# Performance work log

Measured on AMD Instinct MI355X. Metric: run time of the kernel, lower is better.

## Reference

```python
import jax, jax.numpy as jnp
import numpy as np

D_MODEL = 2048
N_HEADS = 32
N_KV_HEADS = 8
HEAD_DIM = D_MODEL // N_HEADS
ROPE_BASE = 10000.0

def setup_inputs() -> dict:
    key = jax.random.key(0)
    ks = jax.random.split(key, 5)
    B, S = 1, 2048
    x = jax.random.normal(ks[0], (B, S, D_MODEL), dtype=jnp.float32)
    sc = 1.0 / np.sqrt(D_MODEL)
    Wq = jax.random.normal(ks[1], (D_MODEL, D_MODEL), dtype=jnp.float32) * sc
    Wk = jax.random.normal(ks[2], (N_KV_HEADS * HEAD_DIM, D_MODEL), dtype=jnp.float32) * sc
    Wv = jax.random.normal(ks[3], (N_KV_HEADS * HEAD_DIM, D_MODEL), dtype=jnp.float32) * sc
    Wo = jax.random.normal(ks[4], (D_MODEL, D_MODEL), dtype=jnp.float32) * sc
    return {"x": x, "Wq": Wq, "Wk": Wk, "Wv": Wv, "Wo": Wo}

def _rope_cos_sin(seq_len, dtype):
    inv_freq = 1.0 / (ROPE_BASE ** (jnp.arange(0, HEAD_DIM, 2, dtype=jnp.float32) / HEAD_DIM))
    t = jnp.arange(seq_len, dtype=jnp.float32)
    freqs = jnp.einsum('i,j->ij', t, inv_freq)          # [S, hd/2]
    emb = jnp.concatenate([freqs, freqs], axis=-1)      # [S, hd]
    return jnp.cos(emb).astype(dtype), jnp.sin(emb).astype(dtype)

def _rotate_half(x):
    x1, x2 = x[..., : HEAD_DIM // 2], x[..., HEAD_DIM // 2 :]
    return jnp.concatenate([-x2, x1], axis=-1)

def reference(x, Wq, Wk, Wv, Wo):
    B, S, _ = x.shape
    scale = HEAD_DIM ** -0.5
    # projections (Linear: x @ W.T)
    q = (x @ Wq.T).reshape(B, S, N_HEADS, HEAD_DIM).transpose(0, 2, 1, 3)      # [B,H,S,hd]
    k = (x @ Wk.T).reshape(B, S, N_KV_HEADS, HEAD_DIM).transpose(0, 2, 1, 3)   # [B,Hkv,S,hd]
    v = (x @ Wv.T).reshape(B, S, N_KV_HEADS, HEAD_DIM).transpose(0, 2, 1, 3)
    cos, sin = _rope_cos_sin(S, x.dtype)                # [S,hd], broadcasts over B,H
    q = q * cos + _rotate_half(q) * sin
    k = k * cos + _rotate_half(k) * sin
    rep = N_HEADS // N_KV_HEADS
    k = jnp.repeat(k, rep, axis=1)                       # [B,H,S,hd]
    v = jnp.repeat(v, rep, axis=1)
    scores = jnp.einsum('bhqd,bhkd->bhqk', q, k) * scale # [B,H,S,S]
    attn = jax.nn.softmax(scores, axis=-1)
    out = jnp.einsum('bhqk,bhkd->bhqd', attn, v)         # [B,H,S,hd]
    out = out.transpose(0, 2, 1, 3).reshape(B, S, D_MODEL)
    return out @ Wo.T
```

## Files before the change

### kernel.cpp

```cpp
#include <hip/hip_runtime.h>
#include <hip/hip_bf16.h>
#include <cmath>

typedef __bf16 bf16_t;
typedef __attribute__((ext_vector_type(8))) __bf16 bf16x8;
typedef __attribute__((ext_vector_type(4))) float f32x4;
typedef __attribute__((ext_vector_type(4))) short s16x4;

#define S_LEN 2048
#define DMODEL 2048
#define KVDIM 512
#define NHEADS 32
#define NKV 8
#define HDIM 64

__device__ inline f32x4 zero4() { f32x4 z; z[0]=0.f; z[1]=0.f; z[2]=0.f; z[3]=0.f; return z; }

__global__ void convert_all(const float* __restrict__ s0, bf16_t* __restrict__ d0,
                            const float* __restrict__ s1, bf16_t* __restrict__ d1,
                            const float* __restrict__ s2, bf16_t* __restrict__ d2,
                            const float* __restrict__ s3, bf16_t* __restrict__ d3,
                            const float* __restrict__ s4, bf16_t* __restrict__ d4) {
  int b = blockIdx.x;
  const float* src; bf16_t* dst; int boff;
  if      (b < 2048) { src = s0; dst = d0; boff = b; }
  else if (b < 4096) { src = s1; dst = d1; boff = b - 2048; }
  else if (b < 4608) { src = s2; dst = d2; boff = b - 4096; }
  else if (b < 5120) { src = s3; dst = d3; boff = b - 4608; }
  else               { src = s4; dst = d4; boff = b - 5120; }
  int idx = (boff * 256 + threadIdx.x) * 8;
  bf16x8 v;
#pragma unroll
  for (int j = 0; j < 8; j++) v[j] = (bf16_t)src[idx + j];
  *(bf16x8*)(dst + idx) = v;
}

template <int BN, bool F32OUT>
__device__ __forceinline__ void gemm_core(const bf16_t* __restrict__ A,
                                          const bf16_t* __restrict__ Bt,
                                          void* __restrict__ Cout,
                                          int N, int K, int bm, int bn) {
  constexpr int NT_W = BN / 32;
  __shared__ __attribute__((aligned(16))) bf16_t As[128 * 64];
  __shared__ __attribute__((aligned(16))) bf16_t Bs[BN * 64];
  const int tid  = threadIdx.x;
  const int wave = tid >> 6, lane = tid & 63;
  const int wm = wave >> 1, wn = wave & 1;
  const int quad = lane >> 4, lr = lane & 15;
  const int srow = lane >> 3, scol = lane & 7;

  f32x4 acc[4][NT_W];
#pragma unroll
  for (int i = 0; i < 4; i++)
#pragma unroll
    for (int j = 0; j < NT_W; j++) acc[i][j] = zero4();

  for (int k0 = 0; k0 < K; k0 += 64) {
#pragma unroll
    for (int i = 0; i < 4; i++) {
      const bf16_t* gA = A + (size_t)(bm + i * 32 + wave * 8 + srow) * K + k0 + scol * 8;
      bf16_t* lA = As + (i * 32 + wave * 8) * 64;
      __builtin_amdgcn_global_load_lds((const __attribute__((address_space(1))) void*)gA,
                                       (__attribute__((address_space(3))) void*)lA, 16, 0, 0);
    }
#pragma unroll
    for (int i = 0; i < BN / 32; i++) {
      const bf16_t* gB = Bt + (size_t)(bn + i * 32 + wave * 8 + srow) * K + k0 + scol * 8;
      bf16_t* lB = Bs + (i * 32 + wave * 8) * 64;
      __builtin_amdgcn_global_load_lds((const __attribute__((address_space(1))) void*)gB,
                                       (__attribute__((address_space(3))) void*)lB, 16, 0, 0);
    }
    __syncthreads();
#pragma unroll
    for (int ks = 0; ks < 2; ks++) {
      bf16x8 a[4], b[NT_W];
#pragma unroll
      for (int mt = 0; mt < 4; mt++)
        a[mt] = *(const bf16x8*)&As[(wm * 64 + mt * 16 + lr) * 64 + ks * 32 + quad * 8];
#pragma unroll
      for (int nt = 0; nt < NT_W; nt++)
        b[nt] = *(const bf16x8*)&Bs[(wn * (BN / 2) + nt * 16 + lr) * 64 + ks * 32 + quad * 8];
#pragma unroll
      for (int mt = 0; mt < 4; mt++)
#pragma unroll
        for (int nt = 0; nt < NT_W; nt++)
          acc[mt][nt] = __builtin_amdgcn_mfma_f32_16x16x32_bf16(a[mt], b[nt], acc[mt][nt], 0, 0, 0);
    }
    __syncthreads();
  }

#pragma unroll
  for (int mt = 0; mt < 4; mt++)
#pragma unroll
    for (int nt = 0; nt < NT_W; nt++)
#pragma unroll
      for (int r = 0; r < 4; r++) {
        int row = bm + wm * 64 + mt * 16 + quad * 4 + r;
        int col = bn + wn * (BN / 2) + nt * 16 + lr;
        if (F32OUT) ((float*)Cout)[(size_t)row * N + col] = acc[mt][nt][r];
        else ((bf16_t*)Cout)[(size_t)row * N + col] = (bf16_t)acc[mt][nt][r];
      }
}

__global__ __launch_bounds__(256) void gemm_proj(const bf16_t* __restrict__ xb,
                                                 const bf16_t* __restrict__ Wqb,
                                                 const bf16_t* __restrict__ Wkb,
                                                 const bf16_t* __restrict__ Wvb,
                                                 bf16_t* __restrict__ qb,
                                                 bf16_t* __restrict__ kb,
                                                 bf16_t* __restrict__ vb) {
  int b = blockIdx.x;
  if (b < 512) {
    gemm_core<64, false>(xb, Wqb, qb, 2048, 2048, (b >> 5) * 128, (b & 31) * 64);
  } else if (b < 640) {
    int r = b - 512;
    gemm_core<64, false>(xb, Wkb, kb, 512, 2048, (r >> 3) * 128, (r & 7) * 64);
  } else {
    int r = b - 640;
    gemm_core<64, false>(Wvb, xb, vb, 2048, 2048, (r >> 5) * 128, (r & 31) * 64);
  }
}

__global__ __launch_bounds__(256) void gemm_out(const bf16_t* __restrict__ A,
                                                const bf16_t* __restrict__ Bt,
                                                float* __restrict__ C) {
  int b = blockIdx.x;
  gemm_core<64, true>(A, Bt, C, 2048, 2048, (b >> 5) * 128, (b & 31) * 64);
}

__global__ void rope_k(bf16_t* __restrict__ kb) {
  int idx = blockIdx.x * 256 + threadIdx.x;
  int s = idx >> 8;
  int rem = idx & 255;
  int head = rem >> 5;
  int i = rem & 31;
  float freq = __expf(-0.2878231366f * (float)i);
  float ang = (float)s * freq;
  float sn, cs;
  sincosf(ang, &sn, &cs);
  size_t base = (size_t)s * KVDIM + head * 64 + i;
  float x0 = (float)kb[base];
  float x1 = (float)kb[base + 32];
  kb[base]      = (bf16_t)(x0 * cs - x1 * sn);
  kb[base + 32] = (bf16_t)(x1 * cs + x0 * sn);
}

__global__ __launch_bounds__(256) void attn_kernel(const bf16_t* __restrict__ q,
                                                   const bf16_t* __restrict__ k,
                                                   const bf16_t* __restrict__ vT,
                                                   bf16_t* __restrict__ out) {
  __shared__ __attribute__((aligned(16))) bf16_t Ks[128 * 64];
  __shared__ __attribute__((aligned(16))) bf16_t Vs[64 * 128];
  const int tid  = threadIdx.x;
  const int wave = tid >> 6, lane = tid & 63;
  const int quad = lane >> 4, lr = lane & 15;
  const int srow = lane >> 3, scol = lane & 7;
  const int vrow = lane >> 4, vcol = lane & 15;
  const int cg = scol ^ srow;
  const int qt = blockIdx.x, h = blockIdx.y;
  const int hkv = h >> 2;
  const int qrow0 = qt * 128 + wave * 32;
  const int sw = lr & 7;
  const int c0 = (quad ^ sw) * 8;
  const int c1 = ((quad + 4) ^ sw) * 8;

  bf16x8 aqA0, aqA1, aqB0, aqB1;
#pragma unroll
  for (int set = 0; set < 2; set++) {
    int row = qrow0 + set * 16 + lr;
    const bf16_t* qp = q + (size_t)row * DMODEL + h * HDIM + quad * 8;
    bf16x8 r0 = *(const bf16x8*)qp;
    bf16x8 r1 = *(const bf16x8*)(qp + 32);
    float srow_f = (float)row;
    bf16x8 a0, a1;
#pragma unroll
    for (int j = 0; j < 8; j++) {
      float freq = __expf(-0.2878231366f * (float)(quad * 8 + j));
      float sn, cs;
      sincosf(srow_f * freq, &sn, &cs);
      float x0 = (float)r0[j], x1 = (float)r1[j];
      a0[j] = (bf16_t)(x0 * cs - x1 * sn);
      a1[j] = (bf16_t)(x1 * cs + x0 * sn);
    }
    if (set == 0) { aqA0 = a0; aqA1 = a1; } else { aqB0 = a0; aqB1 = a1; }
  }

  f32x4 OA[4], OB[4];
  float lA = 0.f, lB = 0.f;
#pragma unroll
  for (int mt = 0; mt < 4; mt++) { OA[mt] = zero4(); OB[mt] = zero4(); }

  for (int kt = 0; kt < S_LEN; kt += 128) {
#pragma unroll
    for (int j = 0; j < 4; j++) {
      const bf16_t* gK = k + (size_t)(kt + wave * 32 + j * 8 + srow) * KVDIM + hkv * HDIM + cg * 8;
      bf16_t* lK = Ks + (wave * 32 + j * 8) * 64;
      __builtin_amdgcn_global_load_lds((const __attribute__((address_space(1))) void*)gK,
                                       (__attribute__((address_space(3))) void*)lK, 16, 0, 0);
    }
#pragma unroll
    for (int j = 0; j < 4; j++) {
      int dg = wave * 16 + j * 4 + vrow;
      int cgv = vcol ^ (dg & 7);
      const bf16_t* gV = vT + (size_t)(hkv * HDIM + dg) * S_LEN + kt + cgv * 8;
      bf16_t* lV = Vs + (wave * 16 + j * 4) * 128;
      __builtin_amdgcn_global_load_lds((const __attribute__((address_space(1))) void*)gV,
                                       (__attribute__((address_space(3))) void*)lV, 16, 0, 0);
    }
    __syncthreads();

    s16x4 bpA[8], bpB[8];
#pragma unroll
    for (int nt = 0; nt < 8; nt++) {
      const int rk = (nt * 16 + lr) * 64;
      bf16x8 kb0 = *(const bf16x8*)&Ks[rk + c0];
      bf16x8 kb1 = *(const bf16x8*)&Ks[rk + c1];
      f32x4 sA = zero4(), sB = zero4();
      sA = __builtin_amdgcn_mfma_f32_16x16x32_bf16(kb0, aqA0, sA, 0, 0, 0);
      sA = __builtin_amdgcn_mfma_f32_16x16x32_bf16(kb1, aqA1, sA, 0, 0, 0);
      sB = __builtin_amdgcn_mfma_f32_16x16x32_bf16(kb0, aqB0, sB, 0, 0, 0);
      sB = __builtin_amdgcn_mfma_f32_16x16x32_bf16(kb1, aqB1, sB, 0, 0, 0);
#pragma unroll
      for (int r = 0; r < 4; r++) {
        float pA = __expf(sA[r] * 0.125f);
        lA += pA;
        bpA[nt][r] = __builtin_bit_cast(short, (bf16_t)pA);
        float pB = __expf(sB[r] * 0.125f);
        lB += pB;
        bpB[nt][r] = __builtin_bit_cast(short, (bf16_t)pB);
      }
    }
#pragma unroll
    for (int nt = 0; nt < 8; nt++) {
      const int slot = ((nt * 2 + (quad >> 1)) ^ sw) * 8 + (quad & 1) * 4;
      s16x4 av[4];
#pragma unroll
      for (int mt = 0; mt < 4; mt++)
        av[mt] = *(const s16x4*)&Vs[(mt * 16 + lr) * 128 + slot];
#pragma unroll
      for (int mt = 0; mt < 4; mt++) {
        OA[mt] = __builtin_amdgcn_mfma_f32_16x16x16bf16_1k(av[mt], bpA[nt], OA[mt], 0, 0, 0);
        OB[mt] = __builtin_amdgcn_mfma_f32_16x16x16bf16_1k(av[mt], bpB[nt], OB[mt], 0, 0, 0);
      }
    }
    __syncthreads();
  }

  lA += __shfl_xor(lA, 16);
  lA += __shfl_xor(lA, 32);
  lB += __shfl_xor(lB, 16);
  lB += __shfl_xor(lB, 32);
  float invA = 1.f / lA;
  float invB = 1.f / lB;

#pragma unroll
  for (int mt = 0; mt < 4; mt++) {
    s16x4 ovA, ovB;
#pragma unroll
    for (int r = 0; r < 4; r++) {
      ovA[r] = __builtin_bit_cast(short, (bf16_t)(OA[mt][r] * invA));
      ovB[r] = __builtin_bit_cast(short, (bf16_t)(OB[mt][r] * invB));
    }
    *(s16x4*)&out[(size_t)(qrow0 + lr) * DMODEL + h * HDIM + mt * 16 + quad * 4] = ovA;
    *(s16x4*)&out[(size_t)(qrow0 + 16 + lr) * DMODEL + h * HDIM + mt * 16 + quad * 4] = ovB;
  }
}

extern "C" void kernel_launch(void* const* d_in, const int* in_sizes, int n_in,
                              void* d_out, int out_size, void* d_ws, size_t ws_size,
                              hipStream_t stream) {
  (void)in_sizes; (void)n_in; (void)out_size; (void)ws_size;
  const float* x  = (const float*)d_in[0];
  const float* Wq = (const float*)d_in[1];
  const float* Wk = (const float*)d_in[2];
  const float* Wv = (const float*)d_in[3];
  const float* Wo = (const float*)d_in[4];

  bf16_t* xb  = (bf16_t*)d_ws;
  bf16_t* Wqb = xb  + (size_t)4 * 1024 * 1024;
  bf16_t* Wkb = Wqb + (size_t)4 * 1024 * 1024;
  bf16_t* Wvb = Wkb + (size_t)1024 * 1024;
  bf16_t* qb  = Wvb + (size_t)1024 * 1024;
  bf16_t* kb  = qb  + (size_t)4 * 1024 * 1024;
  bf16_t* vb  = kb  + (size_t)1024 * 1024;
  bf16_t* Wob = vb  + (size_t)1024 * 1024;
  bf16_t* ab  = xb;

  dim3 blk(256);
  convert_all<<<7168, blk, 0, stream>>>(x, xb, Wq, Wqb, Wk, Wkb, Wv, Wvb, Wo, Wob);
  gemm_proj<<<768, blk, 0, stream>>>(xb, Wqb, Wkb, Wvb, qb, kb, vb);
  rope_k<<<2048, blk, 0, stream>>>(kb);
  attn_kernel<<<dim3(S_LEN / 128, NHEADS), blk, 0, stream>>>(qb, kb, vb, ab);
  gemm_out<<<512, blk, 0, stream>>>(ab, Wob, (float*)d_out);
}
```

Baseline: 237.6 us.

## Split attention key range across two wave groups per block with LDS reduction

The attention kernel now launches 512 threads per block. Two groups of four waves each process half of the key sequence for the same query tile, using separate K/V LDS buffers. At the end, group 1 writes its partial output accumulators and row sums to shared memory, and group 0 adds them before normalising and storing. This doubles waves per block to raise latency hiding on a grid that is small relative to the CU count. In exchange it uses more LDS per block and adds a reduction step and barrier.

Result: slower. 259.9 us (+9.4%).

```diff
diff --git a/kernel.cpp b/kernel.cpp
--- a/kernel.cpp
+++ b/kernel.cpp
@@ -145,21 +145,24 @@
   kb[base + 32] = (bf16_t)(x1 * cs + x0 * sn);
 }
 
-__global__ __launch_bounds__(256) void attn_kernel(const bf16_t* __restrict__ q,
-                                                   const bf16_t* __restrict__ k,
-                                                   const bf16_t* __restrict__ vT,
-                                                   bf16_t* __restrict__ out) {
-  __shared__ __attribute__((aligned(16))) bf16_t Ks[128 * 64];
-  __shared__ __attribute__((aligned(16))) bf16_t Vs[64 * 128];
+__global__ __launch_bounds__(512, 4) void attn_kernel(const bf16_t* __restrict__ q,
+                                                      const bf16_t* __restrict__ k,
+                                                      const bf16_t* __restrict__ vT,
+                                                      bf16_t* __restrict__ out) {
+  __shared__ __attribute__((aligned(16))) bf16_t smem[2 * 128 * 64 + 2 * 64 * 128];
   const int tid  = threadIdx.x;
   const int wave = tid >> 6, lane = tid & 63;
+  const int kw = wave >> 2;
+  const int w4 = wave & 3;
+  bf16_t* Ks = smem + kw * (128 * 64);
+  bf16_t* Vs = smem + 2 * 128 * 64 + kw * (64 * 128);
   const int quad = lane >> 4, lr = lane & 15;
   const int srow = lane >> 3, scol = lane & 7;
   const int vrow = lane >> 4, vcol = lane & 15;
   const int cg = scol ^ srow;
   const int qt = blockIdx.x, h = blockIdx.y;
   const int hkv = h >> 2;
-  const int qrow0 = qt * 128 + wave * 32;
+  const int qrow0 = qt * 128 + w4 * 32;
   const int sw = lr & 7;
   const int c0 = (quad ^ sw) * 8;
   const int c1 = ((quad + 4) ^ sw) * 8;
@@ -190,20 +193,21 @@
 #pragma unroll
   for (int mt = 0; mt < 4; mt++) { OA[mt] = zero4(); OB[mt] = zero4(); }
 
-  for (int kt = 0; kt < S_LEN; kt += 128) {
+  const int kt0 = kw * 1024;
+  for (int kt = kt0; kt < kt0 + 1024; kt += 128) {
 #pragma unroll
     for (int j = 0; j < 4; j++) {
-      const bf16_t* gK = k + (size_t)(kt + wave * 32 + j * 8 + srow) * KVDIM + hkv * HDIM + cg * 8;
-      bf16_t* lK = Ks + (wave * 32 + j * 8) * 64;
+      const bf16_t* gK = k + (size_t)(kt + w4 * 32 + j * 8 + srow) * KVDIM + hkv * HDIM + cg * 8;
+      bf16_t* lK = Ks + (w4 * 32 + j * 8) * 64;
       __builtin_amdgcn_global_load_lds((const __attribute__((address_space(1))) void*)gK,
                                        (__attribute__((address_space(3))) void*)lK, 16, 0, 0);
     }
 #pragma unroll
     for (int j = 0; j < 4; j++) {
-      int dg = wave * 16 + j * 4 + vrow;
+      int dg = w4 * 16 + j * 4 + vrow;
       int cgv = vcol ^ (dg & 7);
       const bf16_t* gV = vT + (size_t)(hkv * HDIM + dg) * S_LEN + kt + cgv * 8;
-      bf16_t* lV = Vs + (wave * 16 + j * 4) * 128;
+      bf16_t* lV = Vs + (w4 * 16 + j * 4) * 128;
       __builtin_amdgcn_global_load_lds((const __attribute__((address_space(1))) void*)gV,
                                        (__attribute__((address_space(3))) void*)lV, 16, 0, 0);
     }
@@ -250,19 +254,44 @@
   lA += __shfl_xor(lA, 32);
   lB += __shfl_xor(lB, 16);
   lB += __shfl_xor(lB, 32);
-  float invA = 1.f / lA;
-  float invB = 1.f / lB;
-
-#pragma unroll
-  for (int mt = 0; mt < 4; mt++) {
-    s16x4 ovA, ovB;
-#pragma unroll
-    for (int r = 0; r < 4; r++) {
-      ovA[r] = __builtin_bit_cast(short, (bf16_t)(OA[mt][r] * invA));
-      ovB[r] = __builtin_bit_cast(short, (bf16_t)(OB[mt][r] * invB));
-    }
-    *(s16x4*)&out[(size_t)(qrow0 + lr) * DMODEL + h * HDIM + mt * 16 + quad * 4] = ovA;
-    *(s16x4*)&out[(size_t)(qrow0 + 16 + lr) * DMODEL + h * HDIM + mt * 16 + quad * 4] = ovB;
+
+  float* fb = (float*)smem;
+  const int cidx = (w4 * 64 + lane) * 35;
+  if (kw == 1) {
+#pragma unroll
+    for (int mt = 0; mt < 4; mt++)
+#pragma unroll
+      for (int r = 0; r < 4; r++) {
+        fb[cidx + mt * 4 + r]      = OA[mt][r];
+        fb[cidx + 16 + mt * 4 + r] = OB[mt][r];
+      }
+    fb[cidx + 32] = lA;
+    fb[cidx + 33] = lB;
+  }
+  __syncthreads();
+  if (kw == 0) {
+#pragma unroll
+    for (int mt = 0; mt < 4; mt++)
+#pragma unroll
+      for (int r = 0; r < 4; r++) {
+        OA[mt][r] += fb[cidx + mt * 4 + r];
+        OB[mt][r] += fb[cidx + 16 + mt * 4 + r];
+      }
+    lA += fb[cidx + 32];
+    lB += fb[cidx + 33];
+    float invA = 1.f / lA;
+    float invB = 1.f / lB;
+#pragma unroll
+    for (int mt = 0; mt < 4; mt++) {
+      s16x4 ovA, ovB;
+#pragma unroll
+      for (int r = 0; r < 4; r++) {
+        ovA[r] = __builtin_bit_cast(short, (bf16_t)(OA[mt][r] * invA));
+        ovB[r] = __builtin_bit_cast(short, (bf16_t)(OB[mt][r] * invB));
+      }
+      *(s16x4*)&out[(size_t)(qrow0 + lr) * DMODEL + h * HDIM + mt * 16 + quad * 4] = ovA;
+      *(s16x4*)&out[(size_t)(qrow0 + 16 + lr) * DMODEL + h * HDIM + mt * 16 + quad * 4] = ovB;
+    }
   }
 }
 
@@ -290,6 +319,6 @@
   convert_all<<<7168, blk, 0, stream>>>(x, xb, Wq, Wqb, Wk, Wkb, Wv, Wvb, Wo, Wob);
   gemm_proj<<<768, blk, 0, stream>>>(xb, Wqb, Wkb, Wvb, qb, kb, vb);
   rope_k<<<2048, blk, 0, stream>>>(kb);
-  attn_kernel<<<dim3(S_LEN / 128, NHEADS), blk, 0, stream>>>(qb, kb, vb, ab);
+  attn_kernel<<<dim3(S_LEN / 128, NHEADS), dim3(512), 0, stream>>>(qb, kb, vb, ab);
   gemm_out<<<512, blk, 0, stream>>>(ab, Wob, (float*)d_out);
 }
```

## Split attention KV range across two blocks and merge partials in combine kernel

Applied to the files above, without the earlier changes.

The attention grid gains a z dimension of 2, so each block covers half the key sequence. Each block writes unnormalized fp32 output partials and row sums into workspace (and into the output buffer as scratch). A new combine kernel adds the partials, normalizes and emits bf16 for the output projection. This doubles block count to improve CU occupancy and latency hiding, at the cost of extra fp32 global traffic and one more launch. It also swaps __expf for a native exp2 with a pre-scaled constant.

After: 250.3 us. 1.05x slower.

```diff
diff --git a/kernel.cpp b/kernel.cpp
--- a/kernel.cpp
+++ b/kernel.cpp
@@ -148,7 +148,9 @@
 __global__ __launch_bounds__(256) void attn_kernel(const bf16_t* __restrict__ q,
                                                    const bf16_t* __restrict__ k,
                                                    const bf16_t* __restrict__ vT,
-                                                   bf16_t* __restrict__ out) {
+                                                   float* __restrict__ Op0,
+                                                   float* __restrict__ Op1,
+                                                   float* __restrict__ l01) {
   __shared__ __attribute__((aligned(16))) bf16_t Ks[128 * 64];
   __shared__ __attribute__((aligned(16))) bf16_t Vs[64 * 128];
   const int tid  = threadIdx.x;
@@ -157,12 +159,14 @@
   const int srow = lane >> 3, scol = lane & 7;
   const int vrow = lane >> 4, vcol = lane & 15;
   const int cg = scol ^ srow;
-  const int qt = blockIdx.x, h = blockIdx.y;
+  const int qt = blockIdx.x, h = blockIdx.y, kw = blockIdx.z;
   const int hkv = h >> 2;
   const int qrow0 = qt * 128 + wave * 32;
   const int sw = lr & 7;
   const int c0 = (quad ^ sw) * 8;
   const int c1 = ((quad + 4) ^ sw) * 8;
+  float* Op = kw ? Op1 : Op0;
+  float* lp = l01 + kw * (S_LEN * NHEADS);
 
   bf16x8 aqA0, aqA1, aqB0, aqB1;
 #pragma unroll
@@ -190,7 +194,8 @@
 #pragma unroll
   for (int mt = 0; mt < 4; mt++) { OA[mt] = zero4(); OB[mt] = zero4(); }
 
-  for (int kt = 0; kt < S_LEN; kt += 128) {
+  const int kt0 = kw * (S_LEN / 2);
+  for (int kt = kt0; kt < kt0 + S_LEN / 2; kt += 128) {
 #pragma unroll
     for (int j = 0; j < 4; j++) {
       const bf16_t* gK = k + (size_t)(kt + wave * 32 + j * 8 + srow) * KVDIM + hkv * HDIM + cg * 8;
@@ -222,10 +227,10 @@
       sB = __builtin_amdgcn_mfma_f32_16x16x32_bf16(kb1, aqB1, sB, 0, 0, 0);
 #pragma unroll
       for (int r = 0; r < 4; r++) {
-        float pA = __expf(sA[r] * 0.125f);
+        float pA = __builtin_amdgcn_exp2f(sA[r] * 0.1803368801f);
         lA += pA;
         bpA[nt][r] = __builtin_bit_cast(short, (bf16_t)pA);
-        float pB = __expf(sB[r] * 0.125f);
+        float pB = __builtin_amdgcn_exp2f(sB[r] * 0.1803368801f);
         lB += pB;
         bpB[nt][r] = __builtin_bit_cast(short, (bf16_t)pB);
       }
@@ -250,20 +255,37 @@
   lA += __shfl_xor(lA, 32);
   lB += __shfl_xor(lB, 16);
   lB += __shfl_xor(lB, 32);
-  float invA = 1.f / lA;
-  float invB = 1.f / lB;
 
 #pragma unroll
   for (int mt = 0; mt < 4; mt++) {
-    s16x4 ovA, ovB;
-#pragma unroll
-    for (int r = 0; r < 4; r++) {
-      ovA[r] = __builtin_bit_cast(short, (bf16_t)(OA[mt][r] * invA));
-      ovB[r] = __builtin_bit_cast(short, (bf16_t)(OB[mt][r] * invB));
-    }
-    *(s16x4*)&out[(size_t)(qrow0 + lr) * DMODEL + h * HDIM + mt * 16 + quad * 4] = ovA;
-    *(s16x4*)&out[(size_t)(qrow0 + 16 + lr) * DMODEL + h * HDIM + mt * 16 + quad * 4] = ovB;
-  }
+    *(f32x4*)&Op[(size_t)(qrow0 + lr) * DMODEL + h * HDIM + mt * 16 + quad * 4] = OA[mt];
+    *(f32x4*)&Op[(size_t)(qrow0 + 16 + lr) * DMODEL + h * HDIM + mt * 16 + quad * 4] = OB[mt];
+  }
+  if (quad == 0) {
+    lp[(qrow0 + lr) * NHEADS + h] = lA;
+    lp[(qrow0 + 16 + lr) * NHEADS + h] = lB;
+  }
+}
+
+__global__ void combine_kernel(const float* __restrict__ O0,
+                               const float* __restrict__ O1,
+                               const float* __restrict__ l01,
+                               bf16_t* __restrict__ ab) {
+  int idx = (blockIdx.x * 256 + threadIdx.x) * 8;
+  int row = idx >> 11;
+  int h = (idx & 2047) >> 6;
+  float inv = 1.f / (l01[row * NHEADS + h] + l01[S_LEN * NHEADS + row * NHEADS + h]);
+  f32x4 a0 = *(const f32x4*)&O0[idx];
+  f32x4 a1 = *(const f32x4*)&O0[idx + 4];
+  f32x4 b0 = *(const f32x4*)&O1[idx];
+  f32x4 b1 = *(const f32x4*)&O1[idx + 4];
+  bf16x8 o;
+#pragma unroll
+  for (int r = 0; r < 4; r++) {
+    o[r]     = (bf16_t)((a0[r] + b0[r]) * inv);
+    o[4 + r] = (bf16_t)((a1[r] + b1[r]) * inv);
+  }
+  *(bf16x8*)&ab[idx] = o;
 }
 
 extern "C" void kernel_launch(void* const* d_in, const int* in_sizes, int n_in,
@@ -284,12 +306,16 @@
   bf16_t* kb  = qb  + (size_t)4 * 1024 * 1024;
   bf16_t* vb  = kb  + (size_t)1024 * 1024;
   bf16_t* Wob = vb  + (size_t)1024 * 1024;
-  bf16_t* ab  = xb;
+  float* Op0 = (float*)d_ws;
+  float* Op1 = (float*)d_out;
+  float* l01 = (float*)Wkb;
+  bf16_t* ab = qb;
 
   dim3 blk(256);
   convert_all<<<7168, blk, 0, stream>>>(x, xb, Wq, Wqb, Wk, Wkb, Wv, Wvb, Wo, Wob);
   gemm_proj<<<768, blk, 0, stream>>>(xb, Wqb, Wkb, Wvb, qb, kb, vb);
   rope_k<<<2048, blk, 0, stream>>>(kb);
-  attn_kernel<<<dim3(S_LEN / 128, NHEADS), blk, 0, stream>>>(qb, kb, vb, ab);
+  attn_kernel<<<dim3(S_LEN / 128, NHEADS, 2), blk, 0, stream>>>(qb, kb, vb, Op0, Op1, l01);
+  combine_kernel<<<2048, blk, 0, stream>>>(Op0, Op1, l01, ab);
   gemm_out<<<512, blk, 0, stream>>>(ab, Wob, (float*)d_out);
 }
```

## Double-buffer K/V tiles in attention and raise MFMA wave priority

Applied to the files above, without the earlier changes.

Doubles the LDS K and V buffers so the next tile's global-to-LDS loads are issued before computing on the current tile, overlapping memory latency with MFMA work and dropping one barrier per iteration. It also wraps MFMA groups in s_setprio to favor matrix issue, and swaps __expf for a direct exp2 with the log2(e) factor folded into the scale. LDS use doubles to 64KB per block, which may reduce occupancy. Correctness relies on the global_load_lds completing before the single __syncthreads at the end of each iteration.

Result: no change. 236.6 us (-0.4%).

```diff
diff --git a/kernel.cpp b/kernel.cpp
--- a/kernel.cpp
+++ b/kernel.cpp
@@ -149,8 +149,8 @@
                                                    const bf16_t* __restrict__ k,
                                                    const bf16_t* __restrict__ vT,
                                                    bf16_t* __restrict__ out) {
-  __shared__ __attribute__((aligned(16))) bf16_t Ks[128 * 64];
-  __shared__ __attribute__((aligned(16))) bf16_t Vs[64 * 128];
+  __shared__ __attribute__((aligned(16))) bf16_t Ks[2][128 * 64];
+  __shared__ __attribute__((aligned(16))) bf16_t Vs[2][64 * 128];
   const int tid  = threadIdx.x;
   const int wave = tid >> 6, lane = tid & 63;
   const int quad = lane >> 4, lr = lane & 15;
@@ -190,42 +190,55 @@
 #pragma unroll
   for (int mt = 0; mt < 4; mt++) { OA[mt] = zero4(); OB[mt] = zero4(); }
 
+#define STAGE_TILE(BUF, KT)                                                              \
+  {                                                                                      \
+    _Pragma("unroll")                                                                    \
+    for (int j = 0; j < 4; j++) {                                                        \
+      const bf16_t* gK = k + (size_t)((KT) + wave * 32 + j * 8 + srow) * KVDIM +         \
+                         hkv * HDIM + cg * 8;                                            \
+      bf16_t* lK = Ks[BUF] + (wave * 32 + j * 8) * 64;                                   \
+      __builtin_amdgcn_global_load_lds((const __attribute__((address_space(1))) void*)gK,\
+                                       (__attribute__((address_space(3))) void*)lK, 16, 0, 0); \
+    }                                                                                    \
+    _Pragma("unroll")                                                                    \
+    for (int j = 0; j < 4; j++) {                                                        \
+      int dg = wave * 16 + j * 4 + vrow;                                                 \
+      int cgv = vcol ^ (dg & 7);                                                         \
+      const bf16_t* gV = vT + (size_t)(hkv * HDIM + dg) * S_LEN + (KT) + cgv * 8;        \
+      bf16_t* lV = Vs[BUF] + (wave * 16 + j * 4) * 128;                                  \
+      __builtin_amdgcn_global_load_lds((const __attribute__((address_space(1))) void*)gV,\
+                                       (__attribute__((address_space(3))) void*)lV, 16, 0, 0); \
+    }                                                                                    \
+  }
+
+  STAGE_TILE(0, 0);
+  __syncthreads();
+
+  int cur = 0;
   for (int kt = 0; kt < S_LEN; kt += 128) {
-#pragma unroll
-    for (int j = 0; j < 4; j++) {
-      const bf16_t* gK = k + (size_t)(kt + wave * 32 + j * 8 + srow) * KVDIM + hkv * HDIM + cg * 8;
-      bf16_t* lK = Ks + (wave * 32 + j * 8) * 64;
-      __builtin_amdgcn_global_load_lds((const __attribute__((address_space(1))) void*)gK,
-                                       (__attribute__((address_space(3))) void*)lK, 16, 0, 0);
-    }
-#pragma unroll
-    for (int j = 0; j < 4; j++) {
-      int dg = wave * 16 + j * 4 + vrow;
-      int cgv = vcol ^ (dg & 7);
-      const bf16_t* gV = vT + (size_t)(hkv * HDIM + dg) * S_LEN + kt + cgv * 8;
-      bf16_t* lV = Vs + (wave * 16 + j * 4) * 128;
-      __builtin_amdgcn_global_load_lds((const __attribute__((address_space(1))) void*)gV,
-                                       (__attribute__((address_space(3))) void*)lV, 16, 0, 0);
-    }
-    __syncthreads();
+    if (kt + 128 < S_LEN) STAGE_TILE(cur ^ 1, kt + 128);
+    const bf16_t* Kc = Ks[cur];
+    const bf16_t* Vc = Vs[cur];
 
     s16x4 bpA[8], bpB[8];
 #pragma unroll
     for (int nt = 0; nt < 8; nt++) {
       const int rk = (nt * 16 + lr) * 64;
-      bf16x8 kb0 = *(const bf16x8*)&Ks[rk + c0];
-      bf16x8 kb1 = *(const bf16x8*)&Ks[rk + c1];
+      bf16x8 kb0 = *(const bf16x8*)&Kc[rk + c0];
+      bf16x8 kb1 = *(const bf16x8*)&Kc[rk + c1];
       f32x4 sA = zero4(), sB = zero4();
+      __builtin_amdgcn_s_setprio(1);
       sA = __builtin_amdgcn_mfma_f32_16x16x32_bf16(kb0, aqA0, sA, 0, 0, 0);
       sA = __builtin_amdgcn_mfma_f32_16x16x32_bf16(kb1, aqA1, sA, 0, 0, 0);
       sB = __builtin_amdgcn_mfma_f32_16x16x32_bf16(kb0, aqB0, sB, 0, 0, 0);
       sB = __builtin_amdgcn_mfma_f32_16x16x32_bf16(kb1, aqB1, sB, 0, 0, 0);
+      __builtin_amdgcn_s_setprio(0);
 #pragma unroll
       for (int r = 0; r < 4; r++) {
-        float pA = __expf(sA[r] * 0.125f);
+        float pA = __builtin_amdgcn_exp2f(sA[r] * 0.1803368801f);
         lA += pA;
         bpA[nt][r] = __builtin_bit_cast(short, (bf16_t)pA);
-        float pB = __expf(sB[r] * 0.125f);
+        float pB = __builtin_amdgcn_exp2f(sB[r] * 0.1803368801f);
         lB += pB;
         bpB[nt][r] = __builtin_bit_cast(short, (bf16_t)pB);
       }
@@ -236,15 +249,19 @@
       s16x4 av[4];
 #pragma unroll
       for (int mt = 0; mt < 4; mt++)
-        av[mt] = *(const s16x4*)&Vs[(mt * 16 + lr) * 128 + slot];
+        av[mt] = *(const s16x4*)&Vc[(mt * 16 + lr) * 128 + slot];
+      __builtin_amdgcn_s_setprio(1);
 #pragma unroll
       for (int mt = 0; mt < 4; mt++) {
         OA[mt] = __builtin_amdgcn_mfma_f32_16x16x16bf16_1k(av[mt], bpA[nt], OA[mt], 0, 0, 0);
         OB[mt] = __builtin_amdgcn_mfma_f32_16x16x16bf16_1k(av[mt], bpB[nt], OB[mt], 0, 0, 0);
       }
+      __builtin_amdgcn_s_setprio(0);
     }
     __syncthreads();
-  }
+    cur ^= 1;
+  }
+#undef STAGE_TILE
 
   lA += __shfl_xor(lA, 16);
   lA += __shfl_xor(lA, 32);
```
